# Kernel tuning notes

Hardware: AMD Instinct MI355X
Metric: run time of the kernel (lower is better)

## Reference

```python
import jax, jax.numpy as jnp
import numpy as np

B, S, NX, NH = 4, 2048, 1024, 16
HD = NX // NH
MASKED_BIAS = -10000.0


def setup_inputs() -> dict:
    key = jax.random.key(0)
    k1, k2, k3 = jax.random.split(key, 3)
    return {
        "hidden_states": jax.random.normal(k1, (B, S, NX), dtype=jnp.float32),
        "c_attn_w": jax.random.normal(k2, (NX, 3 * NX), dtype=jnp.float32) * 0.02,
        "c_attn_b": jnp.zeros((3 * NX,), dtype=jnp.float32),
        "c_proj_w": jax.random.normal(k3, (NX, NX), dtype=jnp.float32) * 0.02,
        "c_proj_b": jnp.zeros((NX,), dtype=jnp.float32),
    }


def reference(hidden_states, c_attn_w, c_attn_b, c_proj_w, c_proj_b):
    b, s, nx = hidden_states.shape
    # fused QKV projection (Conv1D == x @ W + b)
    qkv = hidden_states @ c_attn_w + c_attn_b          # [b, s, 3*nx]
    q, k, v = jnp.split(qkv, 3, axis=-1)
    # split heads -> [b, h, s, d]
    q = q.reshape(b, s, NH, HD).transpose(0, 2, 1, 3)
    k = k.reshape(b, s, NH, HD).transpose(0, 2, 1, 3)
    v = v.reshape(b, s, NH, HD).transpose(0, 2, 1, 3)
    # scaled scores [b, h, s, s]
    w = jnp.einsum("bhqd,bhkd->bhqk", q, k) / jnp.float32(np.sqrt(HD))
    # causal mask via torch.where(mask, w, -10000.0) semantics
    causal = jnp.tril(jnp.ones((s, s), dtype=bool))
    w = jnp.where(causal[None, None], w, jnp.float32(MASKED_BIAS))
    w = jax.nn.softmax(w, axis=-1)
    a = jnp.einsum("bhqk,bhkd->bhqd", w, v)            # [b, h, s, d]
    # merge heads
    a = a.transpose(0, 2, 1, 3).reshape(b, s, nx)
    # output projection
    return a @ c_proj_w + c_proj_b
```

## Files before the change

kernel.cpp:

```cpp
#include <hip/hip_runtime.h>


typedef __bf16 bf16_t;
typedef __bf16 bf16x8 __attribute__((ext_vector_type(8)));
typedef __bf16 bf16x4 __attribute__((ext_vector_type(4)));
typedef float  f32x4  __attribute__((ext_vector_type(4)));

#define DI __device__ __forceinline__

static constexpr int Bq = 4, Sq = 2048, NXq = 1024, NHq = 16, HDq = 64;

DI void gl2lds16(const void* g, void* l) {
#if defined(__has_builtin)
#if __has_builtin(__builtin_amdgcn_global_load_lds)
  __builtin_amdgcn_global_load_lds(
      (const __attribute__((address_space(1))) void*)g,
      (__attribute__((address_space(3))) void*)l, 16, 0, 0);
  return;
#endif
#endif
  *(bf16x8*)l = *(const bf16x8*)g;
}

DI float fast_exp2(float x) {
#if defined(__has_builtin)
#if __has_builtin(__builtin_amdgcn_exp2f)
  return __builtin_amdgcn_exp2f(x);
#else
  return exp2f(x);
#endif
#else
  return exp2f(x);
#endif
}

__global__ __launch_bounds__(256) void cvt_bf16(const float* __restrict__ in,
                                                bf16_t* __restrict__ out, int n) {
  int i = (blockIdx.x * 256 + threadIdx.x) * 4;
  if (i >= n) return;
  float4 v = *(const float4*)(in + i);
  bf16x4 o;
  o[0] = (bf16_t)v.x; o[1] = (bf16_t)v.y; o[2] = (bf16_t)v.z; o[3] = (bf16_t)v.w;
  *(bf16x4*)(out + i) = o;
}

__global__ __launch_bounds__(256) void transpose_cvt(const float* __restrict__ in,
                                                     bf16_t* __restrict__ out,
                                                     int R, int C) {
  __shared__ float t[32][33];
  int bx = blockIdx.x * 32, by = blockIdx.y * 32;
  int tx = threadIdx.x, ty = threadIdx.y;
#pragma unroll
  for (int i = 0; i < 32; i += 8)
    t[ty + i][tx] = in[(size_t)(by + ty + i) * C + bx + tx];
  __syncthreads();
#pragma unroll
  for (int i = 0; i < 32; i += 8)
    out[(size_t)(bx + ty + i) * R + by + tx] = (bf16_t)t[tx][ty + i];
}

DI void gemm_main(const bf16_t* __restrict__ A, const bf16_t* __restrict__ Bt,
                  int K, f32x4 acc[4][4], bf16_t* As, bf16_t* Bs,
                  int lane, int w) {
  const int wy = w >> 1, wx = w & 1;
  const int l15 = lane & 15, quad = lane >> 4;
  for (int kt = 0; kt < K; kt += 32) {
    __syncthreads();
#pragma unroll
    for (int i = 0; i < 2; ++i) {
      int g = w * 2 + i;
      int row = g * 16 + (lane >> 2);
      int ko = kt + (lane & 3) * 8;
      gl2lds16(A + (size_t)row * K + ko, As + g * 512 + lane * 8);
      gl2lds16(Bt + (size_t)row * K + ko, Bs + g * 512 + lane * 8);
    }
    __syncthreads();
    bf16x8 af[4], bfr[4];
#pragma unroll
    for (int mi = 0; mi < 4; ++mi)
      af[mi] = *(const bf16x8*)(As + (wy * 64 + mi * 16 + l15) * 32 + quad * 8);
#pragma unroll
    for (int ni = 0; ni < 4; ++ni)
      bfr[ni] = *(const bf16x8*)(Bs + (wx * 64 + ni * 16 + l15) * 32 + quad * 8);
#pragma unroll
    for (int mi = 0; mi < 4; ++mi)
#pragma unroll
      for (int ni = 0; ni < 4; ++ni)
        acc[mi][ni] = __builtin_amdgcn_mfma_f32_16x16x32_bf16(
            af[mi], bfr[ni], acc[mi][ni], 0, 0, 0);
  }
}

__global__ __launch_bounds__(256) void gemm_qkv(
    const bf16_t* __restrict__ X, const bf16_t* __restrict__ Wt,
    const float* __restrict__ bias, bf16_t* __restrict__ qw,
    bf16_t* __restrict__ kw, bf16_t* __restrict__ vtw) {
  __shared__ __align__(16) bf16_t As[128 * 32];
  __shared__ __align__(16) bf16_t Bs[128 * 32];
  const int tid = threadIdx.x, lane = tid & 63, w = tid >> 6;
  const int m0 = blockIdx.y * 128, n0 = blockIdx.x * 128;
  f32x4 acc[4][4];
#pragma unroll
  for (int mi = 0; mi < 4; ++mi)
#pragma unroll
    for (int ni = 0; ni < 4; ++ni) acc[mi][ni] = (f32x4){0.f, 0.f, 0.f, 0.f};
  gemm_main(X + (size_t)m0 * NXq, Wt + (size_t)n0 * NXq, NXq, acc, As, Bs, lane, w);

  const int wy = w >> 1, wx = w & 1, l15 = lane & 15, quad = lane >> 4;
  const float qscale = 0.125f * 1.44269504088896340736f;
#pragma unroll
  for (int mi = 0; mi < 4; ++mi) {
    int rowb = m0 + wy * 64 + mi * 16 + quad * 4;
    int bb = rowb >> 11, sl = rowb & 2047;
#pragma unroll
    for (int ni = 0; ni < 4; ++ni) {
      int col = n0 + wx * 64 + ni * 16 + l15;
      float bv = bias[col];
      f32x4 v = acc[mi][ni];
      int sec = col >> 10;
      int c = col & 1023;
      int h = c >> 6, d = c & 63;
      if (sec == 0) {
#pragma unroll
        for (int r = 0; r < 4; ++r)
          qw[(((size_t)bb * NHq + h) * Sq + sl + r) * HDq + d] =
              (bf16_t)((v[r] + bv) * qscale);
      } else if (sec == 1) {
#pragma unroll
        for (int r = 0; r < 4; ++r)
          kw[(((size_t)bb * NHq + h) * Sq + sl + r) * HDq + d] = (bf16_t)(v[r] + bv);
      } else {
        bf16x4 t;
#pragma unroll
        for (int r = 0; r < 4; ++r) t[r] = (bf16_t)(v[r] + bv);
        *(bf16x4*)(vtw + (((size_t)bb * NHq + h) * HDq + d) * Sq + sl) = t;
      }
    }
  }
}

__global__ __launch_bounds__(256, 3) void attn_fwd(
    const bf16_t* __restrict__ qw, const bf16_t* __restrict__ kw,
    const bf16_t* __restrict__ vtw, bf16_t* __restrict__ aw) {
  __shared__ __align__(16) bf16_t Ks[2][4096], Vs[2][4096];
  __shared__ __align__(16) bf16_t Ps[4][32 * 72];
  const int tid = threadIdx.x, lane = tid & 63, w = tid >> 6;
  const int l15 = lane & 15, quad = lane >> 4;

  const int id = blockIdx.x;
  const int bh = ((id & 7) << 3) | ((id >> 3) & 7);
  const int k4 = (id >> 6) & 3, quarter = id >> 8;
  int qtile;
  if (quarter == 0)      qtile = 15 - k4;
  else if (quarter == 1) qtile = 8 + k4;
  else if (quarter == 2) qtile = 7 - k4;
  else                   qtile = k4;
  const int b = bh >> 4, h = bh & 15;

  const bf16_t* Qg = qw + ((size_t)bh * Sq + qtile * 128) * HDq;
  const bf16_t* Kg = kw + (size_t)bh * Sq * HDq;
  const bf16_t* Vg = vtw + (size_t)bh * HDq * Sq;

  const int su = w * 2, sr = lane >> 2, sk = (lane & 3) * 8;

#pragma unroll
  for (int i = 0; i < 2; ++i) {
    int u = su + i, p = u >> 2, g = u & 3;
    gl2lds16(Kg + (size_t)(g * 16 + sr) * HDq + p * 32 + sk, Ks[0] + u * 512 + lane * 8);
    gl2lds16(Vg + (size_t)(g * 16 + sr) * Sq + p * 32 + sk, Vs[0] + u * 512 + lane * 8);
  }

  bf16x8 qf[2][2];
#pragma unroll
  for (int mi = 0; mi < 2; ++mi)
#pragma unroll
    for (int ks = 0; ks < 2; ++ks)
      qf[mi][ks] = *(const bf16x8*)(
          Qg + (size_t)((w * 2 + mi) * 16 + l15) * HDq + ks * 32 + quad * 8);

  f32x4 o[2][4];
  float lsum[2][4];
#pragma unroll
  for (int mi = 0; mi < 2; ++mi) {
#pragma unroll
    for (int dt = 0; dt < 4; ++dt) o[mi][dt] = (f32x4){0.f, 0.f, 0.f, 0.f};
#pragma unroll
    for (int r = 0; r < 4; ++r) lsum[mi][r] = 0.f;
  }

  bf16_t* Pw = &Ps[w][0];
  const int jmax = 2 * qtile + 2;
  for (int jt = 0; jt < jmax; ++jt) {
    const int cur = jt & 1;
    __syncthreads();

    if (jt + 1 < jmax) {
      const int nxt = cur ^ 1;
#pragma unroll
      for (int i = 0; i < 2; ++i) {
        int u = su + i, p = u >> 2, g = u & 3;
        gl2lds16(Kg + (size_t)((jt + 1) * 64 + g * 16 + sr) * HDq + p * 32 + sk,
                 Ks[nxt] + u * 512 + lane * 8);
        gl2lds16(Vg + (size_t)(g * 16 + sr) * Sq + (jt + 1) * 64 + p * 32 + sk,
                 Vs[nxt] + u * 512 + lane * 8);
      }
    }

    const bf16_t* Kc = Ks[cur];
    const bf16_t* Vc = Vs[cur];

    f32x4 sc[2][4];
#pragma unroll
    for (int mi = 0; mi < 2; ++mi)
#pragma unroll
      for (int nt = 0; nt < 4; ++nt) sc[mi][nt] = (f32x4){0.f, 0.f, 0.f, 0.f};
#pragma unroll
    for (int ks = 0; ks < 2; ++ks)
#pragma unroll
      for (int nt = 0; nt < 4; ++nt) {
        bf16x8 kf = *(const bf16x8*)(Kc + ks * 2048 + nt * 512 + (l15 * 4 + quad) * 8);
        sc[0][nt] = __builtin_amdgcn_mfma_f32_16x16x32_bf16(qf[0][ks], kf, sc[0][nt], 0, 0, 0);
        sc[1][nt] = __builtin_amdgcn_mfma_f32_16x16x32_bf16(qf[1][ks], kf, sc[1][nt], 0, 0, 0);
      }

    if (jt >= 2 * qtile) {
#pragma unroll
      for (int mi = 0; mi < 2; ++mi) {
        int qrow = qtile * 128 + (w * 2 + mi) * 16 + quad * 4;
#pragma unroll
        for (int nt = 0; nt < 4; ++nt) {
          int key = jt * 64 + nt * 16 + l15;
#pragma unroll
          for (int r = 0; r < 4; ++r)
            if (key > qrow + r) sc[mi][nt][r] = -1e30f;
        }
      }
    }

#pragma unroll
    for (int mi = 0; mi < 2; ++mi)
#pragma unroll
      for (int nt = 0; nt < 4; ++nt)
#pragma unroll
        for (int r = 0; r < 4; ++r) {
          float p = fast_exp2(sc[mi][nt][r]);
          lsum[mi][r] += p;
          Pw[(mi * 16 + quad * 4 + r) * 72 + nt * 16 + l15] = (bf16_t)p;
        }

#pragma unroll
    for (int kk = 0; kk < 2; ++kk) {
      bf16x8 ap0 = *(const bf16x8*)(Pw + (size_t)l15 * 72 + kk * 32 + quad * 8);
      bf16x8 ap1 = *(const bf16x8*)(Pw + (size_t)(16 + l15) * 72 + kk * 32 + quad * 8);
#pragma unroll
      for (int dt = 0; dt < 4; ++dt) {
        bf16x8 bv = *(const bf16x8*)(Vc + kk * 2048 + dt * 512 + (l15 * 4 + quad) * 8);
        o[0][dt] = __builtin_amdgcn_mfma_f32_16x16x32_bf16(ap0, bv, o[0][dt], 0, 0, 0);
        o[1][dt] = __builtin_amdgcn_mfma_f32_16x16x32_bf16(ap1, bv, o[1][dt], 0, 0, 0);
      }
    }
  }

  float linv[2][4];
#pragma unroll
  for (int mi = 0; mi < 2; ++mi)
#pragma unroll
    for (int r = 0; r < 4; ++r) {
      float s = lsum[mi][r];
#pragma unroll
      for (int off = 8; off > 0; off >>= 1) s += __shfl_xor(s, off);
      linv[mi][r] = 1.f / s;
    }

#pragma unroll
  for (int mi = 0; mi < 2; ++mi) {
    int s0 = qtile * 128 + (w * 2 + mi) * 16 + quad * 4;
#pragma unroll
    for (int dt = 0; dt < 4; ++dt) {
      int col = h * 64 + dt * 16 + l15;
#pragma unroll
      for (int r = 0; r < 4; ++r)
        aw[((size_t)b * Sq + s0 + r) * NXq + col] = (bf16_t)(o[mi][dt][r] * linv[mi][r]);
    }
  }
}

__global__ __launch_bounds__(256) void gemm_proj(
    const bf16_t* __restrict__ Aa, const bf16_t* __restrict__ Wt,
    const float* __restrict__ bias, float* __restrict__ out) {
  __shared__ __align__(16) bf16_t As[128 * 32];
  __shared__ __align__(16) bf16_t Bs[128 * 32];
  const int tid = threadIdx.x, lane = tid & 63, w = tid >> 6;
  const int m0 = blockIdx.y * 128, n0 = blockIdx.x * 128;
  f32x4 acc[4][4];
#pragma unroll
  for (int mi = 0; mi < 4; ++mi)
#pragma unroll
    for (int ni = 0; ni < 4; ++ni) acc[mi][ni] = (f32x4){0.f, 0.f, 0.f, 0.f};
  gemm_main(Aa + (size_t)m0 * NXq, Wt + (size_t)n0 * NXq, NXq, acc, As, Bs, lane, w);

  const int wy = w >> 1, wx = w & 1, l15 = lane & 15, quad = lane >> 4;
#pragma unroll
  for (int mi = 0; mi < 4; ++mi) {
    int rowb = m0 + wy * 64 + mi * 16 + quad * 4;
#pragma unroll
    for (int ni = 0; ni < 4; ++ni) {
      int col = n0 + wx * 64 + ni * 16 + l15;
      float bv = bias[col];
#pragma unroll
      for (int r = 0; r < 4; ++r)
        out[(size_t)(rowb + r) * NXq + col] = acc[mi][ni][r] + bv;
    }
  }
}

extern "C" void kernel_launch(void* const* d_in, const int* in_sizes, int n_in,
                              void* d_out, int out_size, void* d_ws, size_t ws_size,
                              hipStream_t stream) {
  const float* hidden   = (const float*)d_in[0];
  const float* c_attn_w = (const float*)d_in[1];
  const float* c_attn_b = (const float*)d_in[2];
  const float* c_proj_w = (const float*)d_in[3];
  const float* c_proj_b = (const float*)d_in[4];
  float* out = (float*)d_out;

  char* ws = (char*)d_ws;
  const size_t szX   = (size_t)8192 * 1024 * 2;
  const size_t szW1  = (size_t)3072 * 1024 * 2;
  const size_t szW2  = (size_t)1024 * 1024 * 2;
  const size_t szQKV = (size_t)Bq * NHq * Sq * HDq * 2;
  bf16_t* Xb  = (bf16_t*)(ws);
  bf16_t* Wt1 = (bf16_t*)(ws + szX);
  bf16_t* Wt2 = (bf16_t*)(ws + szX + szW1);
  bf16_t* qwp = (bf16_t*)(ws + szX + szW1 + szW2);
  bf16_t* kwp = (bf16_t*)(ws + szX + szW1 + szW2 + szQKV);
  bf16_t* vtp = (bf16_t*)(ws + szX + szW1 + szW2 + 2 * szQKV);
  bf16_t* awp = (bf16_t*)(ws + szX + szW1 + szW2 + 3 * szQKV);
  if (ws_size < szX + szW1 + szW2 + 4 * szQKV) return;

  cvt_bf16<<<dim3((8192 * 1024) / (256 * 4)), dim3(256), 0, stream>>>(
      hidden, Xb, 8192 * 1024);
  transpose_cvt<<<dim3(3072 / 32, 1024 / 32), dim3(32, 8), 0, stream>>>(
      c_attn_w, Wt1, 1024, 3072);
  transpose_cvt<<<dim3(1024 / 32, 1024 / 32), dim3(32, 8), 0, stream>>>(
      c_proj_w, Wt2, 1024, 1024);
  gemm_qkv<<<dim3(3072 / 128, 8192 / 128), dim3(256), 0, stream>>>(
      Xb, Wt1, c_attn_b, qwp, kwp, vtp);
  attn_fwd<<<dim3(1024), dim3(256), 0, stream>>>(qwp, kwp, vtp, awp);
  gemm_proj<<<dim3(1024 / 128, 8192 / 128), dim3(256), 0, stream>>>(
      awp, Wt2, c_proj_b, out);
}
```

Before: 257.4 us.

## XOR-swizzle LDS tiles and permute V/P key order to cut bank conflicts

```diff
diff --git a/kernel.cpp b/kernel.cpp
--- a/kernel.cpp
+++ b/kernel.cpp
@@ -64,13 +64,16 @@
                   int lane, int w) {
   const int wy = w >> 1, wx = w & 1;
   const int l15 = lane & 15, quad = lane >> 4;
+  const int sr = lane >> 2;
+  const int sk = 8 * ((lane & 3) ^ ((lane >> 3) & 3));
+  const int qx = quad ^ ((l15 >> 1) & 3);
   for (int kt = 0; kt < K; kt += 32) {
     __syncthreads();
 #pragma unroll
     for (int i = 0; i < 2; ++i) {
       int g = w * 2 + i;
-      int row = g * 16 + (lane >> 2);
-      int ko = kt + (lane & 3) * 8;
+      int row = g * 16 + sr;
+      int ko = kt + sk;
       gl2lds16(A + (size_t)row * K + ko, As + g * 512 + lane * 8);
       gl2lds16(Bt + (size_t)row * K + ko, Bs + g * 512 + lane * 8);
     }
@@ -78,10 +81,10 @@
     bf16x8 af[4], bfr[4];
 #pragma unroll
     for (int mi = 0; mi < 4; ++mi)
-      af[mi] = *(const bf16x8*)(As + (wy * 64 + mi * 16 + l15) * 32 + quad * 8);
+      af[mi] = *(const bf16x8*)(As + (wy * 4 + mi) * 512 + l15 * 32 + qx * 8);
 #pragma unroll
     for (int ni = 0; ni < 4; ++ni)
-      bfr[ni] = *(const bf16x8*)(Bs + (wx * 64 + ni * 16 + l15) * 32 + quad * 8);
+      bfr[ni] = *(const bf16x8*)(Bs + (wx * 4 + ni) * 512 + l15 * 32 + qx * 8);
 #pragma unroll
     for (int mi = 0; mi < 4; ++mi)
 #pragma unroll
@@ -130,10 +133,11 @@
         for (int r = 0; r < 4; ++r)
           kw[(((size_t)bb * NHq + h) * Sq + sl + r) * HDq + d] = (bf16_t)(v[r] + bv);
       } else {
-        bf16x4 t;
-#pragma unroll
-        for (int r = 0; r < 4; ++r) t[r] = (bf16_t)(v[r] + bv);
-        *(bf16x4*)(vtw + (((size_t)bb * NHq + h) * HDq + d) * Sq + sl) = t;
+        int sl64 = sl & 63;
+        int pos0 = (sl & ~63) + ((sl64 & 15) << 2) + (sl64 >> 4);
+        bf16_t* vb = vtw + (((size_t)bb * NHq + h) * HDq + d) * Sq + pos0;
+#pragma unroll
+        for (int r = 0; r < 4; ++r) vb[4 * r] = (bf16_t)(v[r] + bv);
       }
     }
   }
@@ -161,7 +165,9 @@
   const bf16_t* Kg = kw + (size_t)bh * Sq * HDq;
   const bf16_t* Vg = vtw + (size_t)bh * HDq * Sq;
 
-  const int su = w * 2, sr = lane >> 2, sk = (lane & 3) * 8;
+  const int su = w * 2, sr = lane >> 2;
+  const int sk = 8 * ((lane & 3) ^ ((lane >> 3) & 3));
+  const int qx = quad ^ ((l15 >> 1) & 3);
 
 #pragma unroll
   for (int i = 0; i < 2; ++i) {
@@ -218,7 +224,7 @@
     for (int ks = 0; ks < 2; ++ks)
 #pragma unroll
       for (int nt = 0; nt < 4; ++nt) {
-        bf16x8 kf = *(const bf16x8*)(Kc + ks * 2048 + nt * 512 + (l15 * 4 + quad) * 8);
+        bf16x8 kf = *(const bf16x8*)(Kc + (ks * 4 + nt) * 512 + l15 * 32 + qx * 8);
         sc[0][nt] = __builtin_amdgcn_mfma_f32_16x16x32_bf16(qf[0][ks], kf, sc[0][nt], 0, 0, 0);
         sc[1][nt] = __builtin_amdgcn_mfma_f32_16x16x32_bf16(qf[1][ks], kf, sc[1][nt], 0, 0, 0);
       }
@@ -240,13 +246,16 @@
 #pragma unroll
     for (int mi = 0; mi < 2; ++mi)
 #pragma unroll
-      for (int nt = 0; nt < 4; ++nt)
-#pragma unroll
-        for (int r = 0; r < 4; ++r) {
+      for (int r = 0; r < 4; ++r) {
+        bf16x4 pk;
+#pragma unroll
+        for (int nt = 0; nt < 4; ++nt) {
           float p = fast_exp2(sc[mi][nt][r]);
           lsum[mi][r] += p;
-          Pw[(mi * 16 + quad * 4 + r) * 72 + nt * 16 + l15] = (bf16_t)p;
+          pk[nt] = (bf16_t)p;
         }
+        *(bf16x4*)(Pw + (mi * 16 + quad * 4 + r) * 72 + l15 * 4) = pk;
+      }
 
 #pragma unroll
     for (int kk = 0; kk < 2; ++kk) {
@@ -254,7 +263,7 @@
       bf16x8 ap1 = *(const bf16x8*)(Pw + (size_t)(16 + l15) * 72 + kk * 32 + quad * 8);
 #pragma unroll
       for (int dt = 0; dt < 4; ++dt) {
-        bf16x8 bv = *(const bf16x8*)(Vc + kk * 2048 + dt * 512 + (l15 * 4 + quad) * 8);
+        bf16x8 bv = *(const bf16x8*)(Vc + (kk * 4 + dt) * 512 + l15 * 32 + qx * 8);
         o[0][dt] = __builtin_amdgcn_mfma_f32_16x16x32_bf16(ap0, bv, o[0][dt], 0, 0, 0);
         o[1][dt] = __builtin_amdgcn_mfma_f32_16x16x32_bf16(ap1, bv, o[1][dt], 0, 0, 0);
       }
```

Result: slower. 267.2 us (+3.8%).
